# Optimization experiments

Hardware: AMD Instinct MI355X
Metric: run time of the kernel (lower is better)

Reference implementation:

```python
import jax, jax.numpy as jnp
import numpy as np

N = 50000
R = 8
E = 100000
D_IN = 768
D_H = 256
LN_EPS = 1e-5


def _layer_norm(h, g, b):
    mu = jnp.mean(h, axis=-1, keepdims=True)
    var = jnp.mean((h - mu) ** 2, axis=-1, keepdims=True)
    return (h - mu) * jax.lax.rsqrt(var + LN_EPS) * g + b


def _rgcn_layer(x, node_w, edge_src, edge_tgt, W_rel, W_self_w, W_self_b, ln_g, ln_b):
    # x: [N, d_in]; edge_src/edge_tgt: [R, E]; W_rel: [R, d_in, d_out]
    n = x.shape[0]
    out = x @ W_self_w + W_self_b  # self loop
    for r in range(W_rel.shape[0]):  # fixed, small relation count
        src = edge_src[r]
        tgt = edge_tgt[r]
        feats = x[src] * node_w[src][:, None]          # gather + nuclearity scale, [E, d_in]
        msg = feats @ W_rel[r]                          # per-relation linear, [E, d_out]
        agg = jax.ops.segment_sum(msg, tgt, num_segments=n)                 # scatter_add
        cnt = jax.ops.segment_sum(jnp.ones(src.shape[0], x.dtype), tgt, num_segments=n)
        out = out + agg / jnp.clip(cnt, 1.0)[:, None]  # mean over relation neighbors
    return _layer_norm(jax.nn.relu(out), ln_g, ln_b)   # dropout = identity (eval)


def setup_inputs() -> dict:
    key = jax.random.key(0)
    ks = jax.random.split(key, 10)
    x = jax.random.normal(ks[0], (N, D_IN), dtype=jnp.float32)
    node_weights = jax.random.uniform(ks[1], (N,), dtype=jnp.float32)
    edge_src = jax.random.randint(ks[2], (R, E), 0, N, dtype=jnp.int32)
    edge_tgt = jax.random.randint(ks[3], (R, E), 0, N, dtype=jnp.int32)
    W_rel0 = jax.random.normal(ks[4], (R, D_IN, D_H), dtype=jnp.float32) / np.sqrt(D_IN)
    W_self0_w = jax.random.normal(ks[5], (D_IN, D_H), dtype=jnp.float32) / np.sqrt(D_IN)
    W_self0_b = jnp.zeros((D_H,), jnp.float32)
    W_rel1 = jax.random.normal(ks[6], (R, D_H, D_H), dtype=jnp.float32) / np.sqrt(D_H)
    W_self1_w = jax.random.normal(ks[7], (D_H, D_H), dtype=jnp.float32) / np.sqrt(D_H)
    W_self1_b = jnp.zeros((D_H,), jnp.float32)
    ones = jnp.ones((D_H,), jnp.float32)
    zeros = jnp.zeros((D_H,), jnp.float32)
    return {
        "x": x, "node_weights": node_weights,
        "edge_src": edge_src, "edge_tgt": edge_tgt,
        "W_rel0": W_rel0, "W_self0_w": W_self0_w, "W_self0_b": W_self0_b,
        "ln0_g": ones, "ln0_b": zeros,
        "W_rel1": W_rel1, "W_self1_w": W_self1_w, "W_self1_b": W_self1_b,
        "ln1_g": ones, "ln1_b": zeros,
    }


def reference(x, node_weights, edge_src, edge_tgt,
              W_rel0, W_self0_w, W_self0_b, ln0_g, ln0_b,
              W_rel1, W_self1_w, W_self1_b, ln1_g, ln1_b):
    h = _rgcn_layer(x, node_weights, edge_src, edge_tgt,
                    W_rel0, W_self0_w, W_self0_b, ln0_g, ln0_b)
    h = _rgcn_layer(h, node_weights, edge_src, edge_tgt,
                    W_rel1, W_self1_w, W_self1_b, ln1_g, ln1_b)
    return h  # [N, 256]
```

## Files before the change

### kernel.cpp

```cpp
#include <hip/hip_runtime.h>
#include <stdint.h>

#define N_NODES 50000
#define M_PAD   50176
#define R_REL   8
#define E_EDGES 100000
#define D_IN    768
#define D_H     256
#define N_CAT   2304
#define LN_EPS  1e-5f

#define TILES_M256 196
#define TILES_N256 9
#define T_TOT256   1764
#define NCHUNK  49
#define EP_STRIDE 68
#define E_PAD_MAX 960000

typedef __attribute__((ext_vector_type(8))) __bf16        bf16x8;
typedef __attribute__((ext_vector_type(4))) float         f32x4;
typedef __attribute__((ext_vector_type(8))) unsigned short u16x8;
typedef __attribute__((ext_vector_type(4))) unsigned short u16x4;
typedef __attribute__((ext_vector_type(4))) int            i32x4;

__device__ __forceinline__ float bf2f(unsigned short u) {
  union { float f; uint32_t i; } c; c.i = ((uint32_t)u) << 16; return c.f;
}
__device__ __forceinline__ unsigned short f2bf(float f) {
  uint32_t x = __float_as_uint(f);
  uint32_t r = (x + 0x7fffu + ((x >> 16) & 1u)) >> 16;
  return (unsigned short)r;
}

__device__ __forceinline__ void gload_lds16(const void* g, uint32_t lds_off) {
  __builtin_amdgcn_global_load_lds(
      (const __attribute__((address_space(1))) void*)(uintptr_t)g,
      (__attribute__((address_space(3))) void*)(uintptr_t)lds_off, 16, 0, 0);
}

__global__ void k_deg(const int* __restrict__ tgt, int* __restrict__ deg) {
  int e = blockIdx.x * 256 + threadIdx.x;
  if (e >= R_REL * E_EDGES) return;
  int r = e / E_EDGES;
  atomicAdd(&deg[r * N_NODES + tgt[e]], 1);
}

__global__ void k_ndeg(const int* __restrict__ deg, int* __restrict__ pdeg) {
  int t = blockIdx.x * 256 + threadIdx.x;
  if (t >= N_NODES) return;
  int s = 0;
#pragma unroll
  for (int r = 0; r < R_REL; ++r) s += deg[r * N_NODES + t];
  pdeg[t] = (s + 3) & ~3;
}

__global__ __launch_bounds__(256)
void k_scan1(const int* __restrict__ deg, int* __restrict__ rowptr,
             int* __restrict__ bsum) {
  __shared__ int wtot[4];
  const int chunk = blockIdx.x, tid = threadIdx.x;
  const int wave = tid >> 6, lane = tid & 63;
  const int i0 = chunk * 1024 + tid * 4;
  int v0 = 0, v1 = 0, v2 = 0, v3 = 0;
  const int* d = deg;
  if (chunk != NCHUNK - 1) {
    i32x4 v = *(const i32x4*)(d + i0);
    v0 = v[0]; v1 = v[1]; v2 = v[2]; v3 = v[3];
  } else {
    if (i0 + 0 < N_NODES) v0 = d[i0 + 0];
    if (i0 + 1 < N_NODES) v1 = d[i0 + 1];
    if (i0 + 2 < N_NODES) v2 = d[i0 + 2];
    if (i0 + 3 < N_NODES) v3 = d[i0 + 3];
  }
  const int tsum = v0 + v1 + v2 + v3;
  int inc = tsum;
#pragma unroll
  for (int off = 1; off < 64; off <<= 1) {
    int t = __shfl_up(inc, off, 64);
    if (lane >= off) inc += t;
  }
  if (lane == 63) wtot[wave] = inc;
  __syncthreads();
  int woff = 0;
#pragma unroll
  for (int w = 0; w < 4; ++w) woff += (w < wave) ? wtot[w] : 0;
  int excl = woff + inc - tsum;
  int* rp = rowptr;
  if (i0 + 0 < N_NODES) rp[i0 + 0] = excl;
  if (i0 + 1 < N_NODES) rp[i0 + 1] = excl + v0;
  if (i0 + 2 < N_NODES) rp[i0 + 2] = excl + v0 + v1;
  if (i0 + 3 < N_NODES) rp[i0 + 3] = excl + v0 + v1 + v2;
  if (tid == 0) bsum[chunk] = wtot[0] + wtot[1] + wtot[2] + wtot[3];
}

__global__ __launch_bounds__(64)
void k_scan2(const int* __restrict__ bsum, int* __restrict__ chunkoff,
             int* __restrict__ rowptr) {
  const int lane = threadIdx.x & 63;
  int v = (lane < NCHUNK) ? bsum[lane] : 0;
  int inc = v;
#pragma unroll
  for (int off = 1; off < 64; off <<= 1) {
    int t = __shfl_up(inc, off, 64);
    if (lane >= off) inc += t;
  }
  if (lane < NCHUNK) chunkoff[lane] = inc - v;
  if (lane == NCHUNK - 1) rowptr[N_NODES] = inc;
}

__global__ __launch_bounds__(256)
void k_scan3(const int* __restrict__ chunkoff, int* __restrict__ rowptr) {
  const int chunk = blockIdx.x;
  if (chunk == 0) return;
  const int off = chunkoff[chunk];
  const int i0 = chunk * 1024 + threadIdx.x * 4;
#pragma unroll
  for (int j = 0; j < 4; ++j)
    if (i0 + j < N_NODES) rowptr[i0 + j] += off;
}

__global__ void k_prep(const int* __restrict__ nodeptr, int2* __restrict__ scN) {
  int t = blockIdx.x * 256 + threadIdx.x;
  if (t >= N_NODES) return;
  scN[t] = make_int2(nodeptr[t], nodeptr[t + 1] - nodeptr[t]);
}

__global__ void k_fill(const int* __restrict__ src, const int* __restrict__ tgt,
                       const float* __restrict__ nw, const int* __restrict__ nodeptr,
                       const int* __restrict__ deg, int* __restrict__ cursor,
                       int2* __restrict__ e2) {
  int e = blockIdx.x * 256 + threadIdx.x;
  if (e >= R_REL * E_EDGES) return;
  int r = e / E_EDGES;
  int t = tgt[e], s = src[e];
  int pos = atomicAdd(&cursor[t], 1);
  int slot = nodeptr[t] + pos;
  float w = nw[s] / (float)deg[r * N_NODES + t];
  e2[slot] = make_int2(s | (r << 16), __float_as_int(w));
}

__global__ void k_cvt_x(const float* __restrict__ x, unsigned short* __restrict__ xb) {
  const size_t i = ((size_t)blockIdx.x * 256 + threadIdx.x) * 4;
  if (i >= (size_t)N_NODES * D_IN) return;
  const f32x4 v = *(const f32x4*)(x + i);
  u16x4 o = { f2bf(v[0]), f2bf(v[1]), f2bf(v[2]), f2bf(v[3]) };
  *(u16x4*)(xb + i) = o;
}

__global__ void k_cvt_w(const float* __restrict__ Ws, const float* __restrict__ Wr,
                        unsigned short* __restrict__ Wt, int K) {
  int idx = blockIdx.x * 256 + threadIdx.x;
  if (idx >= N_CAT * K) return;
  int n = idx / K, k = idx - n * K;
  float v = (n < 256) ? Ws[k * 256 + n]
                      : Wr[(size_t)((n - 256) >> 8) * K * 256 + k * 256 + (n & 255)];
  Wt[idx] = f2bf(v);
}

__global__ __launch_bounds__(512, 2)
void k_gemm(const unsigned short* __restrict__ A, const unsigned short* __restrict__ Bt,
            unsigned short* __restrict__ C, int K) {
  __shared__ __align__(16) char smem[131072];

  const int bid = blockIdx.x;
  const int xcd = bid & 7, idx = bid >> 3;
  const int q9 = T_TOT256 >> 3, rr = T_TOT256 & 7;
  const int wg = (xcd < rr ? xcd * (q9 + 1)
                           : rr * (q9 + 1) + (xcd - rr) * q9) + idx;
  const int tm9 = wg / 9;
  const int tileM = tm9 * 256;
  const int tileN = (wg - tm9 * 9) * 256;

  const int tid  = threadIdx.x;
  const int wave = tid >> 6, lane = tid & 63;
  const int wmRow = (wave >> 2) * 128;
  const int wnRow = (wave & 3) * 64;
  const int c16 = lane & 15, fph = lane >> 4, x7 = lane & 7;

  const int srow = tid >> 3, sl8 = tid & 7;
  const int cch = sl8 ^ (srow & 7);
  const unsigned short* gA0 = A  + (size_t)(tileM + srow) * K + cch * 8;
  const unsigned short* gB0 = Bt + (size_t)(tileN + srow) * K + cch * 8;
  const uint32_t ldsA = (uint32_t)(uintptr_t)smem;
  const uint32_t ldsB = ldsA + 65536u;
  const uint32_t linA = (uint32_t)(srow * 128 + sl8 * 16);

#define STA(R0, tt) gload_lds16(gA0 + (size_t)(R0) * K + (size_t)(tt) * 64, \
                                ldsA + (uint32_t)(((tt) & 1) * 32768) + (uint32_t)((R0) * 128) + linA)
#define STB(R0, tt) gload_lds16(gB0 + (size_t)(R0) * K + (size_t)(tt) * 64, \
                                ldsB + (uint32_t)(((tt) & 1) * 32768) + (uint32_t)((R0) * 128) + linA)

  f32x4 acc[8][4] = {};

  const char* pA = smem          + (wmRow + c16) * 128;
  const char* pB = smem + 65536  + (wnRow + c16) * 128;

  const int nk = K >> 6;

  STA(0, 0); STA(128, 0); STA(64, 0); STA(192, 0);
  STB(0, 0); STB(64, 0);  STB(128, 0); STB(192, 0);
  STA(0, 1); STA(128, 1);
  asm volatile("s_waitcnt vmcnt(2)" ::: "memory");
  asm volatile("s_barrier" ::: "memory");

  for (int t = 0; t < nk; ++t) {
    const uint32_t bA = (uint32_t)(t & 1) * 32768u;
#pragma unroll
    for (int q = 0; q < 4; ++q) {
      bf16x8 af[2][2], bfr[2][4];
#pragma unroll
      for (int kk = 0; kk < 2; ++kk) {
        const int sA = ((kk * 4 + fph) ^ x7) * 16;
#pragma unroll
        for (int i2 = 0; i2 < 2; ++i2)
          af[i2][kk] = *(const bf16x8*)(pA + bA + (q * 2 + i2) * 2048 + sA);
#pragma unroll
        for (int nj = 0; nj < 4; ++nj)
          bfr[kk][nj] = *(const bf16x8*)(pB + bA + nj * 2048 + sA);
      }
      if (q == 0 && t + 1 < nk) { STA(64, t + 1); STA(192, t + 1); STB(0, t + 1); STB(64, t + 1); }
      if (q == 1 && t + 1 < nk) { STB(128, t + 1); STB(192, t + 1); }
      if (q == 2 && t + 2 < nk) { STA(0, t + 2); STA(128, t + 2); }
      asm volatile("s_barrier" ::: "memory");
      asm volatile("s_waitcnt lgkmcnt(0)" ::: "memory");
      __builtin_amdgcn_s_setprio(1);
#pragma unroll
      for (int i2 = 0; i2 < 2; ++i2)
#pragma unroll
        for (int nj = 0; nj < 4; ++nj)
#pragma unroll
          for (int kk = 0; kk < 2; ++kk)
            acc[q * 2 + i2][nj] = __builtin_amdgcn_mfma_f32_16x16x32_bf16(
                af[i2][kk], bfr[kk][nj], acc[q * 2 + i2][nj], 0, 0, 0);
      __builtin_amdgcn_s_setprio(0);
      if (q < 3) asm volatile("s_barrier" ::: "memory");
    }
    if (t + 1 < nk) {
      if (t + 2 < nk) asm volatile("s_waitcnt vmcnt(2)" ::: "memory");
      else            asm volatile("s_waitcnt vmcnt(0)" ::: "memory");
      asm volatile("s_barrier" ::: "memory");
    }
  }
  asm volatile("s_waitcnt vmcnt(0)" ::: "memory");
  asm volatile("s_barrier" ::: "memory");

#undef STA
#undef STB

  unsigned short* st = (unsigned short*)smem + wave * (64 * EP_STRIDE);
  const int rq4 = (lane >> 4) * 4, cq = lane & 15;
#pragma unroll
  for (int half = 0; half < 2; ++half) {
#pragma unroll
    for (int i = 0; i < 4; ++i)
#pragma unroll
      for (int j = 0; j < 4; ++j)
#pragma unroll
        for (int p = 0; p < 4; ++p)
          st[(i * 16 + rq4 + p) * EP_STRIDE + j * 16 + cq] = f2bf(acc[half * 4 + i][j][p]);
#pragma unroll
    for (int pass = 0; pass < 8; ++pass) {
      const int row = pass * 8 + (lane >> 3);
      const unsigned short* rp_ = st + row * EP_STRIDE + (lane & 7) * 8;
      u16x4 lo = *(const u16x4*)(rp_);
      u16x4 hi = *(const u16x4*)(rp_ + 4);
      u16x8 v = { lo[0], lo[1], lo[2], lo[3], hi[0], hi[1], hi[2], hi[3] };
      size_t off = (size_t)(tileM + wmRow + half * 64 + row) * N_CAT + tileN + wnRow + (lane & 7) * 8;
      *(u16x8*)(C + off) = v;
    }
  }
}

template <int FINAL>
__global__ __launch_bounds__(256)
void k_gather_ln(const unsigned short* __restrict__ Y, const int2* __restrict__ scN,
                 const int2* __restrict__ e2, const float* __restrict__ bias,
                 const float* __restrict__ g, const float* __restrict__ bln,
                 void* __restrict__ out) {
  const int wave = threadIdx.x >> 6, lane = threadIdx.x & 63;
  const int t = blockIdx.x * 4 + wave;
  if (t >= N_NODES) return;
  const int c0 = lane * 4;

  float a0, a1, a2, a3;
  {
    u16x4 sv = *(const u16x4*)(Y + (size_t)t * N_CAT + c0);
    f32x4 bb = *(const f32x4*)(bias + c0);
    a0 = bf2f(sv[0]) + bb[0];
    a1 = bf2f(sv[1]) + bb[1];
    a2 = bf2f(sv[2]) + bb[2];
    a3 = bf2f(sv[3]) + bb[3];
  }

  const int2 s = scN[t];
  const int2* ep = e2 + s.x;
  for (int idx = 0; idx < s.y; idx += 4) {
    const int2 p0 = ep[idx + 0];
    const int2 p1 = ep[idx + 1];
    const int2 p2 = ep[idx + 2];
    const int2 p3 = ep[idx + 3];
    const unsigned short* y0 = Y + (size_t)(p0.x & 0xFFFF) * N_CAT + (((p0.x >> 16) + 1) << 8) + c0;
    const unsigned short* y1 = Y + (size_t)(p1.x & 0xFFFF) * N_CAT + (((p1.x >> 16) + 1) << 8) + c0;
    const unsigned short* y2 = Y + (size_t)(p2.x & 0xFFFF) * N_CAT + (((p2.x >> 16) + 1) << 8) + c0;
    const unsigned short* y3 = Y + (size_t)(p3.x & 0xFFFF) * N_CAT + (((p3.x >> 16) + 1) << 8) + c0;
    u16x4 v0 = *(const u16x4*)y0;
    u16x4 v1 = *(const u16x4*)y1;
    u16x4 v2 = *(const u16x4*)y2;
    u16x4 v3 = *(const u16x4*)y3;
    const float w0 = __int_as_float(p0.y), w1 = __int_as_float(p1.y);
    const float w2 = __int_as_float(p2.y), w3 = __int_as_float(p3.y);
    a0 += w0 * bf2f(v0[0]) + w1 * bf2f(v1[0]) + w2 * bf2f(v2[0]) + w3 * bf2f(v3[0]);
    a1 += w0 * bf2f(v0[1]) + w1 * bf2f(v1[1]) + w2 * bf2f(v2[1]) + w3 * bf2f(v3[1]);
    a2 += w0 * bf2f(v0[2]) + w1 * bf2f(v1[2]) + w2 * bf2f(v2[2]) + w3 * bf2f(v3[2]);
    a3 += w0 * bf2f(v0[3]) + w1 * bf2f(v1[3]) + w2 * bf2f(v2[3]) + w3 * bf2f(v3[3]);
  }

  a0 = fmaxf(a0, 0.f); a1 = fmaxf(a1, 0.f); a2 = fmaxf(a2, 0.f); a3 = fmaxf(a3, 0.f);

  float s1 = (a0 + a1) + (a2 + a3);
#pragma unroll
  for (int off = 32; off > 0; off >>= 1) s1 += __shfl_xor(s1, off, 64);
  const float mu = s1 * (1.f / 256.f);
  const float d0 = a0 - mu, d1 = a1 - mu, d2 = a2 - mu, d3 = a3 - mu;
  float s2 = (d0 * d0 + d1 * d1) + (d2 * d2 + d3 * d3);
#pragma unroll
  for (int off = 32; off > 0; off >>= 1) s2 += __shfl_xor(s2, off, 64);
  const float rs = rsqrtf(s2 * (1.f / 256.f) + LN_EPS);

  f32x4 gg = *(const f32x4*)(g + c0);
  f32x4 ll = *(const f32x4*)(bln + c0);
  const float o0 = d0 * rs * gg[0] + ll[0];
  const float o1 = d1 * rs * gg[1] + ll[1];
  const float o2 = d2 * rs * gg[2] + ll[2];
  const float o3 = d3 * rs * gg[3] + ll[3];
  if (FINAL) {
    f32x4 o = { o0, o1, o2, o3 };
    *(f32x4*)((float*)out + (size_t)t * 256 + c0) = o;
  } else {
    u16x4 o = { f2bf(o0), f2bf(o1), f2bf(o2), f2bf(o3) };
    *(u16x4*)((unsigned short*)out + (size_t)t * 256 + c0) = o;
  }
}

extern "C" void kernel_launch(void* const* d_in, const int* in_sizes, int n_in,
                              void* d_out, int out_size, void* d_ws, size_t ws_size,
                              hipStream_t stream) {
  (void)in_sizes; (void)n_in; (void)out_size; (void)ws_size;
  const float* x   = (const float*)d_in[0];
  const float* nw  = (const float*)d_in[1];
  const int*   esrc = (const int*)d_in[2];
  const int*   etgt = (const int*)d_in[3];
  const float* Wr0 = (const float*)d_in[4];
  const float* Ws0 = (const float*)d_in[5];
  const float* Wb0 = (const float*)d_in[6];
  const float* g0  = (const float*)d_in[7];
  const float* b0  = (const float*)d_in[8];
  const float* Wr1 = (const float*)d_in[9];
  const float* Ws1 = (const float*)d_in[10];
  const float* Wb1 = (const float*)d_in[11];
  const float* g1  = (const float*)d_in[12];
  const float* b1  = (const float*)d_in[13];

  char* p = (char*)d_ws;
  auto carve = [&](size_t bytes) {
    char* q = p;
    p += (bytes + 511) & ~(size_t)511;
    return q;
  };
  unsigned short* Y   = (unsigned short*)carve((size_t)M_PAD * N_CAT * 2);
  unsigned short* xb  = (unsigned short*)carve((size_t)M_PAD * D_IN * 2);
  unsigned short* h   = (unsigned short*)carve((size_t)M_PAD * D_H * 2);
  unsigned short* Wt0 = (unsigned short*)carve((size_t)N_CAT * D_IN * 2);
  unsigned short* Wt1 = (unsigned short*)carve((size_t)N_CAT * D_H * 2);
  int*   deg     = (int*)carve((size_t)R_REL * N_NODES * 4);
  int*   pdeg    = (int*)carve((size_t)N_NODES * 4);
  int*   cursor  = (int*)carve((size_t)N_NODES * 4);
  int*   nodeptr = (int*)carve((size_t)(N_NODES + 1) * 4);
  int*   bsum    = (int*)carve((size_t)NCHUNK * 4);
  int*   chunkoff= (int*)carve((size_t)NCHUNK * 4);
  int2*  e2      = (int2*)carve((size_t)E_PAD_MAX * 8);
  int2*  scN     = (int2*)carve((size_t)N_NODES * 8);

  hipMemsetAsync(deg, 0, (size_t)R_REL * N_NODES * 4, stream);
  hipMemsetAsync(cursor, 0, (size_t)N_NODES * 4, stream);
  hipMemsetAsync(e2, 0, (size_t)E_PAD_MAX * 8, stream);
  k_deg<<<(R_REL * E_EDGES + 255) / 256, 256, 0, stream>>>(etgt, deg);
  k_ndeg<<<(N_NODES + 255) / 256, 256, 0, stream>>>(deg, pdeg);
  k_scan1<<<NCHUNK, 256, 0, stream>>>(pdeg, nodeptr, bsum);
  k_scan2<<<1, 64, 0, stream>>>(bsum, chunkoff, nodeptr);
  k_scan3<<<NCHUNK, 256, 0, stream>>>(chunkoff, nodeptr);
  k_prep<<<(N_NODES + 255) / 256, 256, 0, stream>>>(nodeptr, scN);
  k_fill<<<(R_REL * E_EDGES + 255) / 256, 256, 0, stream>>>(esrc, etgt, nw, nodeptr,
                                                            deg, cursor, e2);
  k_cvt_x<<<(N_NODES * D_IN / 4 + 255) / 256, 256, 0, stream>>>(x, xb);
  k_cvt_w<<<(N_CAT * D_IN + 255) / 256, 256, 0, stream>>>(Ws0, Wr0, Wt0, D_IN);
  k_cvt_w<<<(N_CAT * D_H + 255) / 256, 256, 0, stream>>>(Ws1, Wr1, Wt1, D_H);

  k_gemm<<<T_TOT256, 512, 0, stream>>>(xb, Wt0, Y, D_IN);
  k_gather_ln<0><<<N_NODES / 4, 256, 0, stream>>>(Y, scN, e2, Wb0, g0, b0, h);
  k_gemm<<<T_TOT256, 512, 0, stream>>>(h, Wt1, Y, D_H);
  k_gather_ln<1><<<N_NODES / 4, 256, 0, stream>>>(Y, scN, e2, Wb1, g1, b1, d_out);
}
```

Measured before the change: 827.8 us.

## Keep B fragments in registers per k-tile and prefetch B two tiles ahead

```diff
diff --git a/kernel.cpp b/kernel.cpp
--- a/kernel.cpp
+++ b/kernel.cpp
@@ -199,44 +199,65 @@
 
   STA(0, 0); STA(128, 0); STA(64, 0); STA(192, 0);
   STB(0, 0); STB(64, 0);  STB(128, 0); STB(192, 0);
-  STA(0, 1); STA(128, 1);
-  asm volatile("s_waitcnt vmcnt(2)" ::: "memory");
+  if (nk > 1) {
+    STB(0, 1); STB(64, 1); STB(128, 1); STB(192, 1);
+    STA(0, 1); STA(128, 1);
+    asm volatile("s_waitcnt vmcnt(6)" ::: "memory");
+  } else {
+    asm volatile("s_waitcnt vmcnt(0)" ::: "memory");
+  }
   asm volatile("s_barrier" ::: "memory");
 
   for (int t = 0; t < nk; ++t) {
     const uint32_t bA = (uint32_t)(t & 1) * 32768u;
+    bf16x8 bfr[2][4];
 #pragma unroll
     for (int q = 0; q < 4; ++q) {
-      bf16x8 af[2][2], bfr[2][4];
+      bf16x8 af[2];
 #pragma unroll
       for (int kk = 0; kk < 2; ++kk) {
         const int sA = ((kk * 4 + fph) ^ x7) * 16;
-#pragma unroll
-        for (int i2 = 0; i2 < 2; ++i2)
-          af[i2][kk] = *(const bf16x8*)(pA + bA + (q * 2 + i2) * 2048 + sA);
-#pragma unroll
-        for (int nj = 0; nj < 4; ++nj)
-          bfr[kk][nj] = *(const bf16x8*)(pB + bA + nj * 2048 + sA);
+        af[kk] = *(const bf16x8*)(pA + bA + (q * 2 + 0) * 2048 + sA);
       }
-      if (q == 0 && t + 1 < nk) { STA(64, t + 1); STA(192, t + 1); STB(0, t + 1); STB(64, t + 1); }
-      if (q == 1 && t + 1 < nk) { STB(128, t + 1); STB(192, t + 1); }
-      if (q == 2 && t + 2 < nk) { STA(0, t + 2); STA(128, t + 2); }
+      bf16x8 af1[2];
+#pragma unroll
+      for (int kk = 0; kk < 2; ++kk) {
+        const int sA = ((kk * 4 + fph) ^ x7) * 16;
+        af1[kk] = *(const bf16x8*)(pA + bA + (q * 2 + 1) * 2048 + sA);
+      }
+      if (q == 0) {
+#pragma unroll
+        for (int kk = 0; kk < 2; ++kk) {
+          const int sA = ((kk * 4 + fph) ^ x7) * 16;
+#pragma unroll
+          for (int nj = 0; nj < 4; ++nj)
+            bfr[kk][nj] = *(const bf16x8*)(pB + bA + nj * 2048 + sA);
+        }
+      }
+      if (q == 0 && t + 1 < nk) { STA(64, t + 1); STA(192, t + 1); }
+      if (q == 1 && t + 2 < nk) { STB(0, t + 2); STB(64, t + 2); }
+      if (q == 2 && t + 2 < nk) { STB(128, t + 2); STB(192, t + 2); STA(0, t + 2); STA(128, t + 2); }
+      if (q == 0) asm volatile("s_waitcnt lgkmcnt(8)" ::: "memory");
       asm volatile("s_barrier" ::: "memory");
       asm volatile("s_waitcnt lgkmcnt(0)" ::: "memory");
       __builtin_amdgcn_s_setprio(1);
 #pragma unroll
-      for (int i2 = 0; i2 < 2; ++i2)
-#pragma unroll
-        for (int nj = 0; nj < 4; ++nj)
-#pragma unroll
-          for (int kk = 0; kk < 2; ++kk)
-            acc[q * 2 + i2][nj] = __builtin_amdgcn_mfma_f32_16x16x32_bf16(
-                af[i2][kk], bfr[kk][nj], acc[q * 2 + i2][nj], 0, 0, 0);
+      for (int nj = 0; nj < 4; ++nj)
+#pragma unroll
+        for (int kk = 0; kk < 2; ++kk)
+          acc[q * 2 + 0][nj] = __builtin_amdgcn_mfma_f32_16x16x32_bf16(
+              af[kk], bfr[kk][nj], acc[q * 2 + 0][nj], 0, 0, 0);
+#pragma unroll
+      for (int nj = 0; nj < 4; ++nj)
+#pragma unroll
+        for (int kk = 0; kk < 2; ++kk)
+          acc[q * 2 + 1][nj] = __builtin_amdgcn_mfma_f32_16x16x32_bf16(
+              af1[kk], bfr[kk][nj], acc[q * 2 + 1][nj], 0, 0, 0);
       __builtin_amdgcn_s_setprio(0);
       if (q < 3) asm volatile("s_barrier" ::: "memory");
     }
     if (t + 1 < nk) {
-      if (t + 2 < nk) asm volatile("s_waitcnt vmcnt(2)" ::: "memory");
+      if (t + 2 < nk) asm volatile("s_waitcnt vmcnt(6)" ::: "memory");
       else            asm volatile("s_waitcnt vmcnt(0)" ::: "memory");
       asm volatile("s_barrier" ::: "memory");
     }
```

Measured after the change: 803.2 us. -3.0%, faster.

## Restructure GEMM main loop with unrolled double-buffer and reordered prefetch schedule

Applied to the files above, without the earlier changes.

```diff
diff --git a/kernel.cpp b/kernel.cpp
--- a/kernel.cpp
+++ b/kernel.cpp
@@ -179,73 +179,116 @@
 
   const int srow = tid >> 3, sl8 = tid & 7;
   const int cch = sl8 ^ (srow & 7);
-  const unsigned short* gA0 = A  + (size_t)(tileM + srow) * K + cch * 8;
-  const unsigned short* gB0 = Bt + (size_t)(tileN + srow) * K + cch * 8;
+  const unsigned short* gA = A  + (size_t)(tileM + srow) * K + cch * 8;
+  const unsigned short* gB = Bt + (size_t)(tileN + srow) * K + cch * 8;
+  const unsigned short* gAr0 = gA;
+  const unsigned short* gAr1 = gA + (size_t)64  * K;
+  const unsigned short* gAr2 = gA + (size_t)128 * K;
+  const unsigned short* gAr3 = gA + (size_t)192 * K;
+  const unsigned short* gBr0 = gB;
+  const unsigned short* gBr1 = gB + (size_t)64  * K;
+  const unsigned short* gBr2 = gB + (size_t)128 * K;
+  const unsigned short* gBr3 = gB + (size_t)192 * K;
   const uint32_t ldsA = (uint32_t)(uintptr_t)smem;
   const uint32_t ldsB = ldsA + 65536u;
   const uint32_t linA = (uint32_t)(srow * 128 + sl8 * 16);
 
-#define STA(R0, tt) gload_lds16(gA0 + (size_t)(R0) * K + (size_t)(tt) * 64, \
-                                ldsA + (uint32_t)(((tt) & 1) * 32768) + (uint32_t)((R0) * 128) + linA)
-#define STB(R0, tt) gload_lds16(gB0 + (size_t)(R0) * K + (size_t)(tt) * 64, \
-                                ldsB + (uint32_t)(((tt) & 1) * 32768) + (uint32_t)((R0) * 128) + linA)
+  auto stA = [&](const unsigned short* p, uint32_t rowoff, int du, uint32_t par) {
+    gload_lds16(p + du * 64, ldsA + par * 32768u + rowoff + linA);
+  };
+  auto stB = [&](const unsigned short* p, uint32_t rowoff, int du, uint32_t par) {
+    gload_lds16(p + du * 64, ldsB + par * 32768u + rowoff + linA);
+  };
 
   f32x4 acc[8][4] = {};
 
-  const char* pA = smem          + (wmRow + c16) * 128;
-  const char* pB = smem + 65536  + (wnRow + c16) * 128;
+  const char* pAb = smem         + (wmRow + c16) * 128;
+  const char* pBb = smem + 65536 + (wnRow + c16) * 128;
+  const char* pA0 = pAb + ((fph)     ^ x7) * 16;
+  const char* pA1 = pAb + ((4 + fph) ^ x7) * 16;
+  const char* pB0 = pBb + ((fph)     ^ x7) * 16;
+  const char* pB1 = pBb + ((4 + fph) ^ x7) * 16;
 
   const int nk = K >> 6;
 
-  STA(0, 0); STA(128, 0); STA(64, 0); STA(192, 0);
-  STB(0, 0); STB(64, 0);  STB(128, 0); STB(192, 0);
-  STA(0, 1); STA(128, 1);
-  asm volatile("s_waitcnt vmcnt(2)" ::: "memory");
+  stA(gAr0, 0, 0, 0); stA(gAr1, 8192, 0, 0); stA(gAr2, 16384, 0, 0); stA(gAr3, 24576, 0, 0);
+  stB(gBr0, 0, 0, 0); stB(gBr1, 8192, 0, 0); stB(gBr2, 16384, 0, 0); stB(gBr3, 24576, 0, 0);
+  if (nk > 1) {
+    stB(gBr0, 0, 1, 1); stB(gBr1, 8192, 1, 1); stB(gBr2, 16384, 1, 1); stB(gBr3, 24576, 1, 1);
+    stA(gAr0, 0, 1, 1); stA(gAr2, 16384, 1, 1);
+    asm volatile("s_waitcnt vmcnt(6)" ::: "memory");
+  } else {
+    asm volatile("s_waitcnt vmcnt(0)" ::: "memory");
+  }
   asm volatile("s_barrier" ::: "memory");
 
-  for (int t = 0; t < nk; ++t) {
-    const uint32_t bA = (uint32_t)(t & 1) * 32768u;
-#pragma unroll
-    for (int q = 0; q < 4; ++q) {
-      bf16x8 af[2][2], bfr[2][4];
-#pragma unroll
-      for (int kk = 0; kk < 2; ++kk) {
-        const int sA = ((kk * 4 + fph) ^ x7) * 16;
-#pragma unroll
-        for (int i2 = 0; i2 < 2; ++i2)
-          af[i2][kk] = *(const bf16x8*)(pA + bA + (q * 2 + i2) * 2048 + sA);
-#pragma unroll
-        for (int nj = 0; nj < 4; ++nj)
-          bfr[kk][nj] = *(const bf16x8*)(pB + bA + nj * 2048 + sA);
+#define MM(a, b, c) __builtin_amdgcn_mfma_f32_16x16x32_bf16(a, b, c, 0, 0, 0)
+#define MFMA16(PH, F0, F1, F2, F3)                                                                    \
+  __builtin_amdgcn_s_setprio(1);                                                                      \
+  acc[2*(PH)  ][0] = MM(F0, bk0n0, acc[2*(PH)  ][0]); acc[2*(PH)  ][1] = MM(F0, bk0n1, acc[2*(PH)  ][1]); \
+  acc[2*(PH)  ][2] = MM(F0, bk0n2, acc[2*(PH)  ][2]); acc[2*(PH)  ][3] = MM(F0, bk0n3, acc[2*(PH)  ][3]); \
+  acc[2*(PH)+1][0] = MM(F2, bk0n0, acc[2*(PH)+1][0]); acc[2*(PH)+1][1] = MM(F2, bk0n1, acc[2*(PH)+1][1]); \
+  acc[2*(PH)+1][2] = MM(F2, bk0n2, acc[2*(PH)+1][2]); acc[2*(PH)+1][3] = MM(F2, bk0n3, acc[2*(PH)+1][3]); \
+  acc[2*(PH)  ][0] = MM(F1, bk1n0, acc[2*(PH)  ][0]); acc[2*(PH)  ][1] = MM(F1, bk1n1, acc[2*(PH)  ][1]); \
+  acc[2*(PH)  ][2] = MM(F1, bk1n2, acc[2*(PH)  ][2]); acc[2*(PH)  ][3] = MM(F1, bk1n3, acc[2*(PH)  ][3]); \
+  acc[2*(PH)+1][0] = MM(F3, bk1n0, acc[2*(PH)+1][0]); acc[2*(PH)+1][1] = MM(F3, bk1n1, acc[2*(PH)+1][1]); \
+  acc[2*(PH)+1][2] = MM(F3, bk1n2, acc[2*(PH)+1][2]); acc[2*(PH)+1][3] = MM(F3, bk1n3, acc[2*(PH)+1][3]); \
+  __builtin_amdgcn_s_setprio(0);
+
+  for (int tp = 0; tp < nk; tp += 2) {
+#pragma unroll
+    for (int u = 0; u < 2; ++u) {
+      const int t = tp + u;
+      const uint32_t bA = (uint32_t)u * 32768u;
+      const uint32_t parC = (uint32_t)u;
+      const uint32_t parN = (uint32_t)(1 - u);
+      bf16x8 bk0n0 = *(const bf16x8*)(pB0 + bA + 0*2048);
+      bf16x8 bk1n0 = *(const bf16x8*)(pB1 + bA + 0*2048);
+      bf16x8 bk0n1 = *(const bf16x8*)(pB0 + bA + 1*2048);
+      bf16x8 bk1n1 = *(const bf16x8*)(pB1 + bA + 1*2048);
+      bf16x8 bk0n2 = *(const bf16x8*)(pB0 + bA + 2*2048);
+      bf16x8 bk1n2 = *(const bf16x8*)(pB1 + bA + 2*2048);
+      bf16x8 bk0n3 = *(const bf16x8*)(pB0 + bA + 3*2048);
+      bf16x8 bk1n3 = *(const bf16x8*)(pB1 + bA + 3*2048);
+      bf16x8 a0 = *(const bf16x8*)(pA0 + bA + 0*2048);
+      bf16x8 a1 = *(const bf16x8*)(pA1 + bA + 0*2048);
+      bf16x8 a2 = *(const bf16x8*)(pA0 + bA + 1*2048);
+      bf16x8 a3 = *(const bf16x8*)(pA1 + bA + 1*2048);
+      bf16x8 n0 = *(const bf16x8*)(pA0 + bA + 2*2048);
+      bf16x8 n1 = *(const bf16x8*)(pA1 + bA + 2*2048);
+      bf16x8 n2 = *(const bf16x8*)(pA0 + bA + 3*2048);
+      bf16x8 n3 = *(const bf16x8*)(pA1 + bA + 3*2048);
+      if (t + 1 < nk) { stA(gAr1, 8192, u + 1, parN); stA(gAr3, 24576, u + 1, parN); }
+      MFMA16(0, a0, a1, a2, a3);
+      asm volatile("s_barrier" ::: "memory");
+      a0 = *(const bf16x8*)(pA0 + bA + 4*2048);
+      a1 = *(const bf16x8*)(pA1 + bA + 4*2048);
+      a2 = *(const bf16x8*)(pA0 + bA + 5*2048);
+      a3 = *(const bf16x8*)(pA1 + bA + 5*2048);
+      if (t + 2 < nk) { stB(gBr0, 0, u + 2, parC); stB(gBr1, 8192, u + 2, parC);
+                        stB(gBr2, 16384, u + 2, parC); stB(gBr3, 24576, u + 2, parC); }
+      MFMA16(1, n0, n1, n2, n3);
+      asm volatile("s_barrier" ::: "memory");
+      n0 = *(const bf16x8*)(pA0 + bA + 6*2048);
+      n1 = *(const bf16x8*)(pA1 + bA + 6*2048);
+      n2 = *(const bf16x8*)(pA0 + bA + 7*2048);
+      n3 = *(const bf16x8*)(pA1 + bA + 7*2048);
+      if (t + 2 < nk) { stA(gAr0, 0, u + 2, parC); stA(gAr2, 16384, u + 2, parC); }
+      MFMA16(2, a0, a1, a2, a3);
+      MFMA16(3, n0, n1, n2, n3);
+      if (t + 1 < nk) {
+        if (t + 2 < nk) asm volatile("s_waitcnt vmcnt(6)" ::: "memory");
+        else            asm volatile("s_waitcnt vmcnt(0)" ::: "memory");
+        asm volatile("s_barrier" ::: "memory");
       }
-      if (q == 0 && t + 1 < nk) { STA(64, t + 1); STA(192, t + 1); STB(0, t + 1); STB(64, t + 1); }
-      if (q == 1 && t + 1 < nk) { STB(128, t + 1); STB(192, t + 1); }
-      if (q == 2 && t + 2 < nk) { STA(0, t + 2); STA(128, t + 2); }
-      asm volatile("s_barrier" ::: "memory");
-      asm volatile("s_waitcnt lgkmcnt(0)" ::: "memory");
-      __builtin_amdgcn_s_setprio(1);
-#pragma unroll
-      for (int i2 = 0; i2 < 2; ++i2)
-#pragma unroll
-        for (int nj = 0; nj < 4; ++nj)
-#pragma unroll
-          for (int kk = 0; kk < 2; ++kk)
-            acc[q * 2 + i2][nj] = __builtin_amdgcn_mfma_f32_16x16x32_bf16(
-                af[i2][kk], bfr[kk][nj], acc[q * 2 + i2][nj], 0, 0, 0);
-      __builtin_amdgcn_s_setprio(0);
-      if (q < 3) asm volatile("s_barrier" ::: "memory");
     }
-    if (t + 1 < nk) {
-      if (t + 2 < nk) asm volatile("s_waitcnt vmcnt(2)" ::: "memory");
-      else            asm volatile("s_waitcnt vmcnt(0)" ::: "memory");
-      asm volatile("s_barrier" ::: "memory");
-    }
+    gAr0 += 128; gAr1 += 128; gAr2 += 128; gAr3 += 128;
+    gBr0 += 128; gBr1 += 128; gBr2 += 128; gBr3 += 128;
   }
   asm volatile("s_waitcnt vmcnt(0)" ::: "memory");
   asm volatile("s_barrier" ::: "memory");
-
-#undef STA
-#undef STB
+#undef MFMA16
+#undef MM
 
   unsigned short* st = (unsigned short*)smem + wave * (64 * EP_STRIDE);
   const int rq4 = (lane >> 4) * 4, cq = lane & 15;
```

Result: faster. 783.3 us (-5.4%).
